# Kernel optimization log

Measured on AMD Instinct MI355X. Metric: run time of the kernel, lower is better.

Reference implementation:

```python
import jax, jax.numpy as jnp
import numpy as np

B, S, W, V, E, H, T = 512, 512, 3, 100000, 128, 100, 64
PAD = 0


def setup_inputs() -> dict:
    key = jax.random.key(0)
    ks = jax.random.split(key, 10)
    inputs = jax.random.randint(ks[0], (B, S, W), 0, V)          # word feature ids
    tags = jax.random.randint(ks[1], (B, S), 0, T)
    emb_table = jax.random.normal(ks[2], (V, E), jnp.float32) * 0.1
    W1 = jax.random.normal(ks[3], (E, H), jnp.float32) * (1.0 / np.sqrt(E))
    b1 = jnp.zeros((H,), jnp.float32)
    W2 = jax.random.normal(ks[4], (H, T), jnp.float32) * (1.0 / np.sqrt(H))
    b2 = jnp.zeros((T,), jnp.float32)
    start_trans = jax.random.uniform(ks[5], (T,), jnp.float32, -0.1, 0.1)
    end_trans = jax.random.uniform(ks[6], (T,), jnp.float32, -0.1, 0.1)
    transitions = jax.random.uniform(ks[7], (T, T), jnp.float32, -0.1, 0.1)
    return {"inputs": inputs, "tags": tags, "emb_table": emb_table,
            "W1": W1, "b1": b1, "W2": W2, "b2": b2,
            "start_trans": start_trans, "end_trans": end_trans,
            "transitions": transitions}


def reference(inputs, tags, emb_table, W1, b1, W2, b2,
              start_trans, end_trans, transitions):
    # mask: token is real if any word feature != padding_idx. [S,B] (time-major)
    mask = (jnp.sum(inputs != PAD, axis=-1) != 0).T
    # Emission scorer (dropout disabled = eval/deterministic)
    emb = jnp.take(emb_table, inputs, axis=0).sum(axis=2)        # [B,S,E]
    h = jnp.tanh(emb @ W1 + b1)                                  # [B,S,H]
    em = (h @ W2 + b2).transpose(1, 0, 2)                        # [S,B,T]
    tags_t = tags.T                                              # [S,B]
    maskf = mask.astype(em.dtype)
    b_idx = jnp.arange(em.shape[1])

    # ---- numerator: score of the gold tag path ----
    score = start_trans[tags_t[0]] + em[0, b_idx, tags_t[0]]     # [B]
    trans_sc = transitions[tags_t[:-1], tags_t[1:]]              # [S-1,B]
    em_sc = jnp.take_along_axis(em[1:], tags_t[1:, :, None], axis=2)[..., 0]
    score = score + jnp.sum((trans_sc + em_sc) * maskf[1:], axis=0)
    seq_ends = jnp.sum(mask.astype(jnp.int32), axis=0) - 1       # [B]
    last_tags = tags_t[seq_ends, b_idx]
    numerator = score + end_trans[last_tags]

    # ---- denominator: log partition via forward algorithm (log-semiring scan) ----
    alpha0 = start_trans[None, :] + em[0]                        # [B,T]

    def step(alpha, x):
        em_t, m_t = x                                            # [B,T], [B]
        nxt = jax.nn.logsumexp(
            alpha[:, :, None] + transitions[None, :, :] + em_t[:, None, :],
            axis=1)                                              # [B,T]
        return jnp.where(m_t[:, None], nxt, alpha), None

    alpha, _ = jax.lax.scan(step, alpha0, (em[1:], mask[1:]))
    denominator = jax.nn.logsumexp(alpha + end_trans[None, :], axis=1)

    # loss = -log-likelihood, per batch element (reduce=False)
    return denominator - numerator
```

## Files before the change

### kernel.cpp

```cpp
#include <hip/hip_runtime.h>

#define B_ 512
#define S_ 512
#define E_ 128
#define H_ 100
#define T_ 64
#define V_ 100000
#define BS_ (B_*S_)

typedef __attribute__((ext_vector_type(8))) short bf16x8;
typedef __attribute__((ext_vector_type(4))) float f32x4;
typedef _Float16 h2 __attribute__((ext_vector_type(2)));
union U16x4 { uint4 u; bf16x8 s; };

__device__ __forceinline__ unsigned f2bf1(float x){
    unsigned u = __float_as_uint(x);
    return (u + 0x7FFFu + ((u>>16)&1u)) >> 16;
}
__device__ __forceinline__ float bf2f(unsigned short h){
    return __uint_as_float(((unsigned)h)<<16);
}
__device__ __forceinline__ float rfl_f(float x){
    return __uint_as_float(__builtin_amdgcn_readfirstlane(__float_as_uint(x)));
}
__device__ __forceinline__ unsigned addpack3(unsigned a, unsigned b, unsigned c){
    float lo = __uint_as_float(a<<16) + __uint_as_float(b<<16) + __uint_as_float(c<<16);
    float hi = __uint_as_float(a&0xFFFF0000u) + __uint_as_float(b&0xFFFF0000u)
             + __uint_as_float(c&0xFFFF0000u);
    return f2bf1(lo) | (f2bf1(hi)<<16);
}
__device__ __forceinline__ float fdot2h(unsigned u, h2 e, float c){
    h2 p; __builtin_memcpy(&p, &u, 4);
#if __has_builtin(__builtin_amdgcn_fdot2)
    return __builtin_amdgcn_fdot2(p, e, c, false);
#else
    return fmaf((float)p.x, (float)e.x, fmaf((float)p.y, (float)e.y, c));
#endif
}
__device__ __forceinline__ float dpp_xor1(float x){
    return __int_as_float(__builtin_amdgcn_mov_dpp(__float_as_int(x), 0xB1, 0xF, 0xF, true));
}
__device__ __forceinline__ float dpp_xor2(float x){
    return __int_as_float(__builtin_amdgcn_mov_dpp(__float_as_int(x), 0x4E, 0xF, 0xF, true));
}

__global__ __launch_bounds__(256) void prep_tbl(
    const float* __restrict__ tbl, uint2* __restrict__ tblh)
{
    int idx = blockIdx.x*256 + threadIdx.x;
    if (idx < (V_*E_)/4) {
        float4 v = ((const float4*)tbl)[idx];
        uint2 o;
        o.x = f2bf1(v.x) | (f2bf1(v.y)<<16);
        o.y = f2bf1(v.z) | (f2bf1(v.w)<<16);
        tblh[idx] = o;
    }
}

__global__ __launch_bounds__(64) void prep_w(
    const float* __restrict__ W1, const float* __restrict__ W2,
    uint4* __restrict__ W1f, uint4* __restrict__ W2f)
{
    const int idx = blockIdx.x*64 + threadIdx.x;
    if (idx < 7*4*64) {
        int lane = idx & 63, kt = (idx>>6)&3, nt = idx>>8;
        int n = nt*16 + (lane&15);
        int kb = kt*32 + (lane>>4)*8;
        unsigned wv[4];
        #pragma unroll
        for (int p = 0; p < 4; ++p) {
            float v0 = (n < H_) ? W1[(kb+2*p  )*H_ + n] : 0.f;
            float v1 = (n < H_) ? W1[(kb+2*p+1)*H_ + n] : 0.f;
            wv[p] = f2bf1(v0) | (f2bf1(v1) << 16);
        }
        W1f[idx] = make_uint4(wv[0],wv[1],wv[2],wv[3]);
    } else {
        int id2 = idx - 7*4*64;
        int lane = id2 & 63, kt = (id2>>6)&3, nt = id2>>8;
        int n = nt*16 + (lane&15);
        int kb = kt*32 + (lane>>4)*8;
        unsigned wv[4];
        #pragma unroll
        for (int p = 0; p < 4; ++p) {
            int k0 = kb+2*p, k1 = kb+2*p+1;
            float v0 = (k0 < H_) ? W2[k0*T_ + n] : 0.f;
            float v1 = (k1 < H_) ? W2[k1*T_ + n] : 0.f;
            wv[p] = f2bf1(v0) | (f2bf1(v1) << 16);
        }
        W2f[id2] = make_uint4(wv[0],wv[1],wv[2],wv[3]);
    }
}

__global__ __launch_bounds__(256, 2)
void fused_kernel(
    const int* __restrict__ inputs, const int* __restrict__ tags,
    const unsigned short* __restrict__ tblh,
    const float* __restrict__ b1, const float* __restrict__ b2,
    const uint4* __restrict__ W1f, const uint4* __restrict__ W2f,
    const float* __restrict__ start_trans, const float* __restrict__ end_trans,
    const float* __restrict__ trans, float* __restrict__ out)
{
    __shared__ uint4 sW1f[1792];
    __shared__ uint4 sW2f[1024];
    __shared__ __align__(16) unsigned short ring[2][8][512];
    __shared__ uint4 sA2[2][256];
    __shared__ _Float16 sTrans[T_*T_];
    __shared__ __align__(16) _Float16 pbufH[2][T_];
    __shared__ float pubB[T_];
    __shared__ float fnum[2];
    __shared__ int   icnt[2];
    __shared__ float lsB_sh;
    __shared__ int   prodF[2];
    __shared__ int   consF[2];

    const int b   = blockIdx.x;
    const int tid = threadIdx.x;
    const int wid = tid >> 6;
    const int j   = tid & 63;
    const int d   = wid & 1;
    const bool isProd = wid >= 2;
    const int col = j & 15;
    const int hi  = j >> 4;
    const int rowin = hi * 4;
    const int* tags_b = tags + b*S_;
    const int* in_b   = inputs + (size_t)b*S_*3;

    for (int i = tid; i < 1792; i += 256) sW1f[i] = W1f[i];
    for (int i = tid; i < 1024; i += 256) sW2f[i] = W2f[i];
    for (int i = tid; i < T_*T_; i += 256) sTrans[i] = (_Float16)trans[i];
    if (tid == 0) { prodF[0] = prodF[1] = 0; consF[0] = consF[1] = 0; }

    unsigned long long mball[4];
    #pragma unroll
    for (int g4 = 0; g4 < 4; ++g4) {
        int t = (d*4 + g4)*64 + j;
        int a0 = in_b[t*3+0], a1 = in_b[t*3+1], a2 = in_b[t*3+2];
        mball[g4] = __ballot((a0 | a1 | a2) != 0);
    }
    if (isProd) {
        int cnt = 0;
        #pragma unroll
        for (int g4 = 0; g4 < 4; ++g4) cnt += __popcll(mball[g4]);
        if (j == 0) icnt[d] = cnt;
    }

    __syncthreads();

    auto baseOf = [&](int p){ return d ? (496 - 16*p) : 16*p; };

    float aF = 0.f, lsF = 0.f;

    if (isProd) {
        float bv1[7], bv2[4];
        #pragma unroll
        for (int nt = 0; nt < 7; ++nt) { int n = nt*16+col; bv1[nt] = (n < H_) ? b1[n] : 0.f; }
        #pragma unroll
        for (int nt2 = 0; nt2 < 4; ++nt2) bv2[nt2] = b2[nt2*16+col];
        const float stj = start_trans[j];

        auto issueGathers = [&](int i0, int i1, int i2, uint4* g){
            const unsigned short* tr0 = tblh + (size_t)i0*E_;
            const unsigned short* tr1 = tblh + (size_t)i1*E_;
            const unsigned short* tr2 = tblh + (size_t)i2*E_;
            #pragma unroll
            for (int kt = 0; kt < 4; ++kt) {
                int off = kt*32 + hi*8;
                g[kt*3+0] = *(const uint4*)(tr0 + off);
                g[kt*3+1] = *(const uint4*)(tr1 + off);
                g[kt*3+2] = *(const uint4*)(tr2 + off);
            }
        };

        uint4 g[12];
        int n0, n1, n2;
        float np = 0.f;
        {
            int t = baseOf(0) + col;
            int c0 = in_b[t*3+0], c1 = in_b[t*3+1], c2 = in_b[t*3+2];
            issueGathers(c0, c1, c2, g);
            int t1 = baseOf(1) + col;
            n0 = in_b[t1*3+0]; n1 = in_b[t1*3+1]; n2 = in_b[t1*3+2];
        }

        for (int p = 0; p < 16; ++p) {
            int tpv = 0, tcv = 0;
            if (j < 16) {
                int t = baseOf(p) + j;
                int tm = (t > 0) ? t - 1 : 0;
                tpv = tags_b[tm]; tcv = tags_b[t];
            }

            U16x4 a4[4];
            #pragma unroll
            for (int kt = 0; kt < 4; ++kt)
                a4[kt].u = make_uint4(
                    addpack3(g[kt*3+0].x, g[kt*3+1].x, g[kt*3+2].x),
                    addpack3(g[kt*3+0].y, g[kt*3+1].y, g[kt*3+2].y),
                    addpack3(g[kt*3+0].z, g[kt*3+1].z, g[kt*3+2].z),
                    addpack3(g[kt*3+0].w, g[kt*3+1].w, g[kt*3+2].w));

            if (p < 15) issueGathers(n0, n1, n2, g);
            if (p < 14) {
                int t = baseOf(p+2) + col;
                n0 = in_b[t*3+0]; n1 = in_b[t*3+1]; n2 = in_b[t*3+2];
            }

            f32x4 acc1[7];
            #pragma unroll
            for (int nt = 0; nt < 7; ++nt) {
                f32x4 c; c[0]=bv1[nt]; c[1]=bv1[nt]; c[2]=bv1[nt]; c[3]=bv1[nt];
                #pragma unroll
                for (int k = 0; k < 4; ++k) {
                    U16x4 bfr; bfr.u = sW1f[(nt*4+k)*64 + j];
                    c = __builtin_amdgcn_mfma_f32_16x16x32_bf16(a4[k].s, bfr.s, c, 0,0,0);
                }
                acc1[nt] = c;
            }
            #pragma unroll
            for (int nt = 0; nt < 7; ++nt)
                #pragma unroll
                for (int rr = 0; rr < 4; ++rr) {
                    float x = acc1[nt][rr];
                    acc1[nt][rr] = 1.f - 2.f/(__expf(2.f*x)+1.f);
                }

            if (j >= 32) sA2[d][3*64 + j] = make_uint4(0,0,0,0);
            unsigned short* A2h = (unsigned short*)sA2[d];
            #pragma unroll
            for (int nt = 0; nt < 7; ++nt)
                #pragma unroll
                for (int rr = 0; rr < 4; ++rr) {
                    int k2 = nt*16 + col;
                    int kt2 = k2 >> 5, g2 = (k2>>3)&3, i2v = k2&7;
                    int u4idx = kt2*64 + g2*16 + (rowin + rr);
                    A2h[u4idx*8 + i2v] = (unsigned short)f2bf1(acc1[nt][rr]);
                }
            __builtin_amdgcn_wave_barrier();

            U16x4 a2[4];
            #pragma unroll
            for (int k = 0; k < 4; ++k) a2[k].u = sA2[d][k*64 + j];
            __builtin_amdgcn_wave_barrier();

            unsigned short* tbuf = (unsigned short*)sA2[d];
            #pragma unroll
            for (int nt2 = 0; nt2 < 4; ++nt2) {
                f32x4 c; c[0]=bv2[nt2]; c[1]=bv2[nt2]; c[2]=bv2[nt2]; c[3]=bv2[nt2];
                #pragma unroll
                for (int k = 0; k < 4; ++k) {
                    U16x4 bfr; bfr.u = sW2f[(nt2*4+k)*64 + j];
                    c = __builtin_amdgcn_mfma_f32_16x16x32_bf16(a2[k].s, bfr.s, c, 0,0,0);
                }
                #pragma unroll
                for (int rr = 0; rr < 4; ++rr)
                    tbuf[(rowin+rr)*72 + nt2*16 + col] = (unsigned short)f2bf1(c[rr]);
            }
            __builtin_amdgcn_wave_barrier();

            if (p >= 4) {
                volatile int* cf = &consF[d];
                while (*cf < 2*p - 7) __builtin_amdgcn_s_sleep(1);
                __asm__ volatile("" ::: "memory");
            }
            {
                const int rl = j >> 2;
                const int ch = (j & 3) * 2;
                const uint4* t4 = (const uint4*)tbuf;
                uint4 u0 = t4[rl*9 + ch];
                uint4 u1 = t4[rl*9 + ch + 1];
                int row = baseOf(p) + rl;
                int grp = row >> 3;
                int kidx = d ? (63 - grp) : grp;
                uint4* dst = (uint4*)&ring[d][kidx & 7][(row & 7)*64];
                dst[ch]   = u0;
                dst[ch+1] = u1;
            }
            __asm__ volatile("s_waitcnt lgkmcnt(0)" ::: "memory");
            if (j == 0) prodF[d] = 2*p + 2;
            __builtin_amdgcn_wave_barrier();

            if (j < 16) {
                int t = baseOf(p) + j;
                if (t >= 1) {
                    int word = (t >> 6) - d*4;
                    if ((mball[word] >> (t & 63)) & 1ull) {
                        int grp = t >> 3;
                        int kidx = d ? (63 - grp) : grp;
                        np += (float)sTrans[tpv*T_ + tcv]
                            + bf2f(ring[d][kidx & 7][(t & 7)*64 + tcv]);
                    }
                }
            }
            if (d == 0 && p == 0) {
                int tag0 = __shfl(tcv, 0);
                float term = __shfl(stj, tag0) + bf2f(ring[0][0][tag0]);
                if (j == 0) np += term;
            }
        }

        #pragma unroll
        for (int off = 32; off >= 1; off >>= 1) np += __shfl_xor(np, off, 64);
        if (j == 0) fnum[d] = np;

    } else {
        const int qg  = j >> 2;
        const int qm  = j & 3;
        const bool qb0 = (j & 1) != 0;
        const bool qb1 = (j & 2) != 0;

        h2 E2[32];
        #pragma unroll
        for (int o = 0; o < 4; ++o)
            #pragma unroll
            for (int i = 0; i < 8; ++i) {
                int r0, c0, r1, c1;
                if (d == 0) { r0 = 16*qm + 2*i; c0 = 4*qg + o; r1 = r0 + 1; c1 = c0; }
                else        { r0 = 4*qg + o; c0 = 16*qm + 2*i; r1 = r0; c1 = c0 + 1; }
                h2 e; e.x = (_Float16)__expf(trans[r0*T_ + c0]);
                      e.y = (_Float16)__expf(trans[r1*T_ + c1]);
                E2[o*8 + i] = e;
            }
        if (d == 0) mball[0] &= ~1ull;

        volatile int* pf = &prodF[d];
        while (*pf < 1) __builtin_amdgcn_s_sleep(1);
        __asm__ volatile("" ::: "memory");

        float a, ls;
        if (d == 0) {
            float x0v = start_trans[j] + bf2f(ring[0][0][j]);
            ls = rfl_f(x0v);
            a  = __expf(x0v - ls);
        } else {
            a  = __expf(end_trans[j]);
            ls = 0.f;
        }
        float eg[8];
        #pragma unroll
        for (int s = 0; s < 8; ++s)
            eg[s] = __expf(bf2f(ring[d][0][(d ? (7-s) : s)*64 + j]));

        for (int k = 0; k < 32; ++k) {
            unsigned short raw16[8];
            if (k < 31) {
                while (*pf < k + 2) __builtin_amdgcn_s_sleep(1);
                __asm__ volatile("" ::: "memory");
                const unsigned short* nxt = ring[d][(k+1) & 7];
                #pragma unroll
                for (int s = 0; s < 8; ++s)
                    raw16[s] = nxt[(d ? (7-s) : s)*64 + j];
                __asm__ volatile("s_waitcnt lgkmcnt(0)" ::: "memory");
                if (j == 0) consF[d] = k + 1;
            }
            const int ag = d ? (63 - k) : k;
            const unsigned mg = (unsigned)((mball[(ag>>3) - d*4] >> ((ag&7)*8)) & 0xFFull);

            #pragma unroll
            for (int s = 0; s < 8; ++s) {
                float wv = (d == 0) ? a : (eg[s] * a);
                pbufH[d][j] = (_Float16)(wv * 0.015625f);
                __builtin_amdgcn_wave_barrier();
                float sc   = rfl_f(a);
                float sinv = __builtin_amdgcn_rcpf(sc);
                float logs = __logf(sc);
                float keep = a * sinv;
                float dmul = ((d == 0) ? (eg[s] * sinv) : sinv) * 64.0f;

                const uint4* ph = (const uint4*)pbufH[d];
                uint4 U0 = ph[2*qm];
                uint4 U1 = ph[2*qm + 1];
                float p0, p1, p2, p3;
                p0 = fdot2h(U0.x, E2[ 0], 0.f);  p0 = fdot2h(U0.y, E2[ 1], p0);
                p0 = fdot2h(U0.z, E2[ 2], p0);   p0 = fdot2h(U0.w, E2[ 3], p0);
                p0 = fdot2h(U1.x, E2[ 4], p0);   p0 = fdot2h(U1.y, E2[ 5], p0);
                p0 = fdot2h(U1.z, E2[ 6], p0);   p0 = fdot2h(U1.w, E2[ 7], p0);
                p1 = fdot2h(U0.x, E2[ 8], 0.f);  p1 = fdot2h(U0.y, E2[ 9], p1);
                p1 = fdot2h(U0.z, E2[10], p1);   p1 = fdot2h(U0.w, E2[11], p1);
                p1 = fdot2h(U1.x, E2[12], p1);   p1 = fdot2h(U1.y, E2[13], p1);
                p1 = fdot2h(U1.z, E2[14], p1);   p1 = fdot2h(U1.w, E2[15], p1);
                p2 = fdot2h(U0.x, E2[16], 0.f);  p2 = fdot2h(U0.y, E2[17], p2);
                p2 = fdot2h(U0.z, E2[18], p2);   p2 = fdot2h(U0.w, E2[19], p2);
                p2 = fdot2h(U1.x, E2[20], p2);   p2 = fdot2h(U1.y, E2[21], p2);
                p2 = fdot2h(U1.z, E2[22], p2);   p2 = fdot2h(U1.w, E2[23], p2);
                p3 = fdot2h(U0.x, E2[24], 0.f);  p3 = fdot2h(U0.y, E2[25], p3);
                p3 = fdot2h(U0.z, E2[26], p3);   p3 = fdot2h(U0.w, E2[27], p3);
                p3 = fdot2h(U1.x, E2[28], p3);   p3 = fdot2h(U1.y, E2[29], p3);
                p3 = fdot2h(U1.z, E2[30], p3);   p3 = fdot2h(U1.w, E2[31], p3);

                float t0 = qb1 ? p2 : p0;
                float t1 = qb1 ? p3 : p1;
                float s0 = qb1 ? p0 : p2;
                float s1 = qb1 ? p1 : p3;
                t0 += dpp_xor2(s0);
                t1 += dpp_xor2(s1);
                float tt = qb0 ? t1 : t0;
                float ss = qb0 ? t0 : t1;
                float y  = tt + dpp_xor1(ss);

                float cand = y * dmul;
                const int bit = (d == 0) ? s : (7 - s);
                a = ((mg >> bit) & 1u) ? cand : keep;
                ls += logs;
                __builtin_amdgcn_wave_barrier();
            }
            if (k < 31) {
                #pragma unroll
                for (int s = 0; s < 8; ++s) eg[s] = __expf(bf2f(raw16[s]));
            }
        }

        if (d == 1) {
            pubB[j] = a;
            if (j == 0) lsB_sh = ls;
        } else {
            aF = a; lsF = ls;
        }
    }

    __syncthreads();

    if (wid == 0) {
        float x = aF * pubB[j];
        #pragma unroll
        for (int off = 32; off >= 1; off >>= 1) x += __shfl_xor(x, off, 64);
        int mcount = icnt[0] + icnt[1];
        int se = mcount - 1; if (se < 0) se = 0;
        const int last_tag = tags_b[se];
        float numer = fnum[0] + fnum[1] + end_trans[last_tag];
        if (j == 0) out[b] = lsF + lsB_sh + __logf(x) - numer;
    }
}

extern "C" void kernel_launch(void* const* d_in, const int* in_sizes, int n_in,
                              void* d_out, int out_size, void* d_ws, size_t ws_size,
                              hipStream_t stream) {
    const int*   inputs      = (const int*)  d_in[0];
    const int*   tags        = (const int*)  d_in[1];
    const float* emb_table   = (const float*)d_in[2];
    const float* W1          = (const float*)d_in[3];
    const float* b1          = (const float*)d_in[4];
    const float* W2          = (const float*)d_in[5];
    const float* b2          = (const float*)d_in[6];
    const float* start_trans = (const float*)d_in[7];
    const float* end_trans   = (const float*)d_in[8];
    const float* transitions = (const float*)d_in[9];
    float* out = (float*)d_out;

    unsigned short* tblh = (unsigned short*)d_ws;
    uint4* W1f = (uint4*)((char*)d_ws + (size_t)V_*E_*2);
    uint4* W2f = W1f + 7*4*64;

    prep_tbl<<<dim3((V_*E_/4 + 255)/256), dim3(256), 0, stream>>>(emb_table, (uint2*)tblh);
    prep_w<<<dim3((7*4*64 + 4*4*64)/64), dim3(64), 0, stream>>>(W1, W2, W1f, W2f);
    fused_kernel<<<dim3(B_), dim3(256), 0, stream>>>(
        inputs, tags, tblh, b1, b2, W1f, W2f,
        start_trans, end_trans, transitions, out);
}
```

Baseline: 205.8 us.

## Split CRF scan: producer waves compute middle segment as matrix products via MFMA

The forward-backward scan previously ran all 512 steps on the two consumer waves. Now the consumers handle only the outer 128 steps from each end. The producer waves, once their emissions are computed, accumulate the middle-segment transfer matrices (exp(trans)·diag(exp(em))) as bf16 MFMA matrix products with periodic max-normalisation. The final combine multiplies the forward and backward vectors through these matrices. This shortens the serial dependent chain and uses otherwise idle producer time, at the cost of extra MFMA work, bf16 precision loss in the matrix products, and more shared memory.

```diff
diff --git a/kernel.cpp b/kernel.cpp
--- a/kernel.cpp
+++ b/kernel.cpp
@@ -6,7 +6,6 @@
 #define H_ 100
 #define T_ 64
 #define V_ 100000
-#define BS_ (B_*S_)
 
 typedef __attribute__((ext_vector_type(8))) short bf16x8;
 typedef __attribute__((ext_vector_type(4))) float f32x4;
@@ -36,6 +35,9 @@
 #else
     return fmaf((float)p.x, (float)e.x, fmaf((float)p.y, (float)e.y, c));
 #endif
+}
+__device__ __forceinline__ unsigned pk2bf(float lo, float hi){
+    return __builtin_amdgcn_perm(__float_as_uint(hi), __float_as_uint(lo), 0x07060302u);
 }
 __device__ __forceinline__ float dpp_xor1(float x){
     return __int_as_float(__builtin_amdgcn_mov_dpp(__float_as_int(x), 0xB1, 0xF, 0xF, true));
@@ -102,12 +104,14 @@
 {
     __shared__ uint4 sW1f[1792];
     __shared__ uint4 sW2f[1024];
-    __shared__ __align__(16) unsigned short ring[2][8][512];
+    __shared__ __align__(16) unsigned short ring[2][4][512];
     __shared__ uint4 sA2[2][256];
-    __shared__ _Float16 sTrans[T_*T_];
+    __shared__ __align__(16) unsigned short SBm[2][64*72];
+    __shared__ float mrowL[2][16];
     __shared__ __align__(16) _Float16 pbufH[2][T_];
     __shared__ float pubB[T_];
     __shared__ float fnum[2];
+    __shared__ float lgS[2];
     __shared__ int   icnt[2];
     __shared__ float lsB_sh;
     __shared__ int   prodF[2];
@@ -127,7 +131,6 @@
 
     for (int i = tid; i < 1792; i += 256) sW1f[i] = W1f[i];
     for (int i = tid; i < 1024; i += 256) sW2f[i] = W2f[i];
-    for (int i = tid; i < T_*T_; i += 256) sTrans[i] = (_Float16)trans[i];
     if (tid == 0) { prodF[0] = prodF[1] = 0; consF[0] = consF[1] = 0; }
 
     unsigned long long mball[4];
@@ -149,6 +152,8 @@
     auto baseOf = [&](int p){ return d ? (496 - 16*p) : 16*p; };
 
     float aF = 0.f, lsF = 0.f;
+    float aBv = 0.f, lsBv = 0.f;
+    float v1g = 0.f;
 
     if (isProd) {
         float bv1[7], bv2[4];
@@ -157,6 +162,37 @@
         #pragma unroll
         for (int nt2 = 0; nt2 < 4; ++nt2) bv2[nt2] = b2[nt2*16+col];
         const float stj = start_trans[j];
+
+        uint4 Afr[8];
+        #pragma unroll
+        for (int ti = 0; ti < 4; ++ti)
+            #pragma unroll
+            for (int kt = 0; kt < 2; ++kt) {
+                unsigned w[4];
+                #pragma unroll
+                for (int p = 0; p < 4; ++p) {
+                    int row = ti*16 + col;
+                    int k = kt*32 + hi*8 + 2*p;
+                    float v0, v1;
+                    if (d == 0) { v0 = __expf(trans[k*T_ + row]); v1 = __expf(trans[(k+1)*T_ + row]); }
+                    else        { v0 = __expf(trans[row*T_ + k]); v1 = __expf(trans[row*T_ + k+1]); }
+                    w[p] = f2bf1(v0) | (f2bf1(v1) << 16);
+                }
+                Afr[ti*2+kt] = make_uint4(w[0],w[1],w[2],w[3]);
+            }
+
+        unsigned short* SBd = SBm[d];
+        if (d == 0) {
+            uint4* rp = (uint4*)(SBd + j*72);
+            #pragma unroll
+            for (int q = 0; q < 9; ++q) rp[q] = make_uint4(0,0,0,0);
+            SBd[j*72 + j] = 0x3F80;
+            __builtin_amdgcn_wave_barrier();
+        }
+
+        f32x4 Cm[16];
+        float lg = 0.f;
+        int ncnt = 0;
 
         auto issueGathers = [&](int i0, int i1, int i2, uint4* g){
             const unsigned short* tr0 = tblh + (size_t)i0*E_;
@@ -183,11 +219,13 @@
         }
 
         for (int p = 0; p < 16; ++p) {
-            int tpv = 0, tcv = 0;
+            const int base_p = baseOf(p);
+            int tpv = 0, tcv = 0; float trv = 0.f;
             if (j < 16) {
-                int t = baseOf(p) + j;
+                int t = base_p + j;
                 int tm = (t > 0) ? t - 1 : 0;
                 tpv = tags_b[tm]; tcv = tags_b[t];
+                trv = trans[tpv*T_ + tcv];
             }
 
             U16x4 a4[4];
@@ -198,7 +236,6 @@
                     addpack3(g[kt*3+0].y, g[kt*3+1].y, g[kt*3+2].y),
                     addpack3(g[kt*3+0].z, g[kt*3+1].z, g[kt*3+2].z),
                     addpack3(g[kt*3+0].w, g[kt*3+1].w, g[kt*3+2].w));
-
             if (p < 15) issueGathers(n0, n1, n2, g);
             if (p < 14) {
                 int t = baseOf(p+2) + col;
@@ -257,50 +294,232 @@
             }
             __builtin_amdgcn_wave_barrier();
 
-            if (p >= 4) {
-                volatile int* cf = &consF[d];
-                while (*cf < 2*p - 7) __builtin_amdgcn_s_sleep(1);
-                __asm__ volatile("" ::: "memory");
-            }
-            {
-                const int rl = j >> 2;
-                const int ch = (j & 3) * 2;
-                const uint4* t4 = (const uint4*)tbuf;
-                uint4 u0 = t4[rl*9 + ch];
-                uint4 u1 = t4[rl*9 + ch + 1];
-                int row = baseOf(p) + rl;
-                int grp = row >> 3;
-                int kidx = d ? (63 - grp) : grp;
-                uint4* dst = (uint4*)&ring[d][kidx & 7][(row & 7)*64];
-                dst[ch]   = u0;
-                dst[ch+1] = u1;
-            }
-            __asm__ volatile("s_waitcnt lgkmcnt(0)" ::: "memory");
-            if (j == 0) prodF[d] = 2*p + 2;
-            __builtin_amdgcn_wave_barrier();
+            if (p < 8) {
+                if (p >= 2) {
+                    volatile int* cf = &consF[d];
+                    while (*cf < 2*p - 3) __builtin_amdgcn_s_sleep(1);
+                    __asm__ volatile("" ::: "memory");
+                }
+                {
+                    const int rl = j >> 2;
+                    const int ch = (j & 3) * 2;
+                    const uint4* t4 = (const uint4*)tbuf;
+                    uint4 u0 = t4[rl*9 + ch];
+                    uint4 u1 = t4[rl*9 + ch + 1];
+                    int row = base_p + rl;
+                    int grp = row >> 3;
+                    int kidx = d ? (63 - grp) : grp;
+                    uint4* dst = (uint4*)&ring[d][kidx & 3][(row & 7)*64];
+                    dst[ch]   = u0;
+                    dst[ch+1] = u1;
+                }
+                __asm__ volatile("s_waitcnt lgkmcnt(0)" ::: "memory");
+                if (j == 0) prodF[d] = 2*p + 2;
+                __builtin_amdgcn_wave_barrier();
+            }
 
             if (j < 16) {
-                int t = baseOf(p) + j;
+                int t = base_p + j;
                 if (t >= 1) {
                     int word = (t >> 6) - d*4;
-                    if ((mball[word] >> (t & 63)) & 1ull) {
-                        int grp = t >> 3;
-                        int kidx = d ? (63 - grp) : grp;
-                        np += (float)sTrans[tpv*T_ + tcv]
-                            + bf2f(ring[d][kidx & 7][(t & 7)*64 + tcv]);
-                    }
+                    if ((mball[word] >> (t & 63)) & 1ull)
+                        np += trv + bf2f(tbuf[j*72 + tcv]);
                 }
             }
             if (d == 0 && p == 0) {
                 int tag0 = __shfl(tcv, 0);
-                float term = __shfl(stj, tag0) + bf2f(ring[0][0][tag0]);
+                float term = __shfl(stj, tag0) + bf2f(tbuf[tag0]);
                 if (j == 0) np += term;
             }
+
+            if (p >= 8) {
+                {
+                    int r_ = j >> 2, sg = j & 3;
+                    float mx0 = -1e30f;
+                    #pragma unroll
+                    for (int q = 0; q < 16; ++q)
+                        mx0 = fmaxf(mx0, bf2f(tbuf[r_*72 + sg*16 + q]));
+                    mx0 = fmaxf(mx0, dpp_xor1(mx0));
+                    mx0 = fmaxf(mx0, dpp_xor2(mx0));
+                    if (sg == 0) mrowL[d][r_] = mx0;
+                    __builtin_amdgcn_wave_barrier();
+                }
+                const unsigned long long mbw = mball[(base_p >> 6) - d*4];
+
+                if (d == 1) {
+                    if (p == 8) {
+                        #pragma unroll
+                        for (int ti = 0; ti < 4; ++ti)
+                            #pragma unroll
+                            for (int nt = 0; nt < 4; ++nt)
+                                #pragma unroll
+                                for (int r2 = 0; r2 < 4; ++r2)
+                                    Cm[ti*4+nt][r2] = (ti*16 + 4*hi + r2 == nt*16 + col) ? 1.f : 0.f;
+                    } else {
+                        #pragma unroll
+                        for (int ti = 0; ti < 4; ++ti)
+                            #pragma unroll
+                            for (int nt = 0; nt < 4; ++nt) {
+                                uint2 v = *(const uint2*)(SBd + (nt*16+col)*72 + ti*16 + 4*hi);
+                                Cm[ti*4+nt][0] = bf2f((unsigned short)(v.x & 0xFFFFu));
+                                Cm[ti*4+nt][1] = bf2f((unsigned short)(v.x >> 16));
+                                Cm[ti*4+nt][2] = bf2f((unsigned short)(v.y & 0xFFFFu));
+                                Cm[ti*4+nt][3] = bf2f((unsigned short)(v.y >> 16));
+                            }
+                    }
+                }
+
+                for (int si = 0; si < 16; ++si) {
+                    int t = d ? (base_p + 15 - si) : (base_p + si);
+                    if (!((mbw >> (t & 63)) & 1ull)) continue;
+                    int tr = t - base_p;
+                    float mrv = mrowL[d][tr];
+                    float ev[16];
+                    #pragma unroll
+                    for (int ti = 0; ti < 4; ++ti) {
+                        uint2 e2 = *(const uint2*)(tbuf + tr*72 + ti*16 + 4*hi);
+                        ev[ti*4+0] = __expf(bf2f((unsigned short)(e2.x & 0xFFFFu)) - mrv);
+                        ev[ti*4+1] = __expf(bf2f((unsigned short)(e2.x >> 16)) - mrv);
+                        ev[ti*4+2] = __expf(bf2f((unsigned short)(e2.y & 0xFFFFu)) - mrv);
+                        ev[ti*4+3] = __expf(bf2f((unsigned short)(e2.y >> 16)) - mrv);
+                    }
+                    lg += mrv;
+                    ++ncnt;
+                    const bool donorm = ((ncnt & 7) == 0);
+
+                    if (d == 0) {
+                        uint4 Bf[8];
+                        #pragma unroll
+                        for (int nt = 0; nt < 4; ++nt)
+                            #pragma unroll
+                            for (int kt = 0; kt < 2; ++kt)
+                                Bf[nt*2+kt] = *(const uint4*)(SBd + (nt*16+col)*72 + kt*32 + hi*8);
+                        __builtin_amdgcn_wave_barrier();
+                        f32x4 Ct[16];
+                        #pragma unroll
+                        for (int ti = 0; ti < 4; ++ti)
+                            #pragma unroll
+                            for (int nt = 0; nt < 4; ++nt) {
+                                f32x4 c = {0.f,0.f,0.f,0.f};
+                                U16x4 af; U16x4 bfm;
+                                af.u = Afr[ti*2+0]; bfm.u = Bf[nt*2+0];
+                                c = __builtin_amdgcn_mfma_f32_16x16x32_bf16(af.s, bfm.s, c, 0,0,0);
+                                af.u = Afr[ti*2+1]; bfm.u = Bf[nt*2+1];
+                                c = __builtin_amdgcn_mfma_f32_16x16x32_bf16(af.s, bfm.s, c, 0,0,0);
+                                Ct[ti*4+nt] = c;
+                            }
+                        #pragma unroll
+                        for (int ti = 0; ti < 4; ++ti)
+                            #pragma unroll
+                            for (int nt = 0; nt < 4; ++nt)
+                                #pragma unroll
+                                for (int r2 = 0; r2 < 4; ++r2)
+                                    Ct[ti*4+nt][r2] *= ev[ti*4+r2];
+                        if (donorm) {
+                            float mx = 0.f;
+                            #pragma unroll
+                            for (int q = 0; q < 16; ++q)
+                                #pragma unroll
+                                for (int r2 = 0; r2 < 4; ++r2)
+                                    mx = fmaxf(mx, fabsf(Ct[q][r2]));
+                            #pragma unroll
+                            for (int off = 32; off >= 1; off >>= 1)
+                                mx = fmaxf(mx, __shfl_xor(mx, off, 64));
+                            float inv = 1.f / mx;
+                            #pragma unroll
+                            for (int q = 0; q < 16; ++q)
+                                #pragma unroll
+                                for (int r2 = 0; r2 < 4; ++r2)
+                                    Ct[q][r2] *= inv;
+                            lg += __logf(mx);
+                        }
+                        __builtin_amdgcn_wave_barrier();
+                        #pragma unroll
+                        for (int ti = 0; ti < 4; ++ti)
+                            #pragma unroll
+                            for (int nt = 0; nt < 4; ++nt) {
+                                unsigned w0 = pk2bf(Ct[ti*4+nt][0], Ct[ti*4+nt][1]);
+                                unsigned w1 = pk2bf(Ct[ti*4+nt][2], Ct[ti*4+nt][3]);
+                                *(uint2*)(SBd + (nt*16+col)*72 + ti*16 + 4*hi) = make_uint2(w0, w1);
+                            }
+                        __builtin_amdgcn_wave_barrier();
+                    } else {
+                        f32x4 Ct[16];
+                        #pragma unroll
+                        for (int ti = 0; ti < 4; ++ti)
+                            #pragma unroll
+                            for (int nt = 0; nt < 4; ++nt)
+                                #pragma unroll
+                                for (int r2 = 0; r2 < 4; ++r2)
+                                    Ct[ti*4+nt][r2] = Cm[ti*4+nt][r2] * ev[ti*4+r2];
+                        if (donorm) {
+                            float mx = 0.f;
+                            #pragma unroll
+                            for (int q = 0; q < 16; ++q)
+                                #pragma unroll
+                                for (int r2 = 0; r2 < 4; ++r2)
+                                    mx = fmaxf(mx, fabsf(Ct[q][r2]));
+                            #pragma unroll
+                            for (int off = 32; off >= 1; off >>= 1)
+                                mx = fmaxf(mx, __shfl_xor(mx, off, 64));
+                            float inv = 1.f / mx;
+                            #pragma unroll
+                            for (int q = 0; q < 16; ++q)
+                                #pragma unroll
+                                for (int r2 = 0; r2 < 4; ++r2)
+                                    Ct[q][r2] *= inv;
+                            lg += __logf(mx);
+                        }
+                        __builtin_amdgcn_wave_barrier();
+                        #pragma unroll
+                        for (int ti = 0; ti < 4; ++ti)
+                            #pragma unroll
+                            for (int nt = 0; nt < 4; ++nt) {
+                                unsigned w0 = pk2bf(Ct[ti*4+nt][0], Ct[ti*4+nt][1]);
+                                unsigned w1 = pk2bf(Ct[ti*4+nt][2], Ct[ti*4+nt][3]);
+                                *(uint2*)(SBd + (nt*16+col)*72 + ti*16 + 4*hi) = make_uint2(w0, w1);
+                            }
+                        __builtin_amdgcn_wave_barrier();
+                        uint4 Bf[8];
+                        #pragma unroll
+                        for (int nt = 0; nt < 4; ++nt)
+                            #pragma unroll
+                            for (int kt = 0; kt < 2; ++kt)
+                                Bf[nt*2+kt] = *(const uint4*)(SBd + (nt*16+col)*72 + kt*32 + hi*8);
+                        __builtin_amdgcn_wave_barrier();
+                        #pragma unroll
+                        for (int ti = 0; ti < 4; ++ti)
+                            #pragma unroll
+                            for (int nt = 0; nt < 4; ++nt) {
+                                f32x4 c = {0.f,0.f,0.f,0.f};
+                                U16x4 af; U16x4 bfm;
+                                af.u = Afr[ti*2+0]; bfm.u = Bf[nt*2+0];
+                                c = __builtin_amdgcn_mfma_f32_16x16x32_bf16(af.s, bfm.s, c, 0,0,0);
+                                af.u = Afr[ti*2+1]; bfm.u = Bf[nt*2+1];
+                                c = __builtin_amdgcn_mfma_f32_16x16x32_bf16(af.s, bfm.s, c, 0,0,0);
+                                Cm[ti*4+nt] = c;
+                            }
+                    }
+                }
+
+                if (d == 1) {
+                    __builtin_amdgcn_wave_barrier();
+                    #pragma unroll
+                    for (int ti = 0; ti < 4; ++ti)
+                        #pragma unroll
+                        for (int nt = 0; nt < 4; ++nt) {
+                            unsigned w0 = pk2bf(Cm[ti*4+nt][0], Cm[ti*4+nt][1]);
+                            unsigned w1 = pk2bf(Cm[ti*4+nt][2], Cm[ti*4+nt][3]);
+                            *(uint2*)(SBd + (nt*16+col)*72 + ti*16 + 4*hi) = make_uint2(w0, w1);
+                        }
+                    __builtin_amdgcn_wave_barrier();
+                }
+            }
         }
 
         #pragma unroll
         for (int off = 32; off >= 1; off >>= 1) np += __shfl_xor(np, off, 64);
-        if (j == 0) fnum[d] = np;
+        if (j == 0) { fnum[d] = np; lgS[d] = lg; }
 
     } else {
         const int qg  = j >> 2;
@@ -340,12 +559,12 @@
         for (int s = 0; s < 8; ++s)
             eg[s] = __expf(bf2f(ring[d][0][(d ? (7-s) : s)*64 + j]));
 
-        for (int k = 0; k < 32; ++k) {
+        for (int k = 0; k < 16; ++k) {
             unsigned short raw16[8];
-            if (k < 31) {
+            if (k < 15) {
                 while (*pf < k + 2) __builtin_amdgcn_s_sleep(1);
                 __asm__ volatile("" ::: "memory");
-                const unsigned short* nxt = ring[d][(k+1) & 7];
+                const unsigned short* nxt = ring[d][(k+1) & 3];
                 #pragma unroll
                 for (int s = 0; s < 8; ++s)
                     raw16[s] = nxt[(d ? (7-s) : s)*64 + j];
@@ -403,31 +622,51 @@
                 ls += logs;
                 __builtin_amdgcn_wave_barrier();
             }
-            if (k < 31) {
+            if (k < 15) {
                 #pragma unroll
                 for (int s = 0; s < 8; ++s) eg[s] = __expf(bf2f(raw16[s]));
             }
         }
 
-        if (d == 1) {
-            pubB[j] = a;
-            if (j == 0) lsB_sh = ls;
-        } else {
-            aF = a; lsF = ls;
-        }
+        if (d == 0) { aF = a; lsF = ls; }
+        else        { aBv = a; lsBv = ls; }
     }
 
     __syncthreads();
 
     if (wid == 0) {
-        float x = aF * pubB[j];
+        float* aBuf = (float*)&ring[0][0][0];
+        aBuf[j] = aF;
+        __builtin_amdgcn_wave_barrier();
+        const unsigned short* P0 = SBm[0];
+        float v1 = 0.f;
+        #pragma unroll 8
+        for (int i = 0; i < 64; ++i)
+            v1 += aBuf[i] * bf2f(P0[i*72 + j]);
+        v1g = v1;
+    } else if (wid == 1) {
+        float* bBuf = (float*)&ring[1][0][0];
+        bBuf[j] = aBv;
+        __builtin_amdgcn_wave_barrier();
+        const unsigned short* Q0 = SBm[1];
+        float v2 = 0.f;
+        #pragma unroll 8
+        for (int i = 0; i < 64; ++i)
+            v2 += bBuf[i] * bf2f(Q0[i*72 + j]);
+        pubB[j] = v2;
+        if (j == 0) lsB_sh = lsBv;
+    }
+    __syncthreads();
+
+    if (wid == 0) {
+        float x = v1g * pubB[j];
         #pragma unroll
         for (int off = 32; off >= 1; off >>= 1) x += __shfl_xor(x, off, 64);
         int mcount = icnt[0] + icnt[1];
         int se = mcount - 1; if (se < 0) se = 0;
         const int last_tag = tags_b[se];
         float numer = fnum[0] + fnum[1] + end_trans[last_tag];
-        if (j == 0) out[b] = lsF + lsB_sh + __logf(x) - numer;
+        if (j == 0) out[b] = lsF + lsB_sh + lgS[0] + lgS[1] + __logf(x) - numer;
     }
 }
 
```

Result: slower. 544.7 us (+164.7%).
